# Performance work log

Hardware: AMD Instinct MI355X
Metric: run time of the kernel (lower is better)

The kernel has to match this reference:

```python
import jax, jax.numpy as jnp
import numpy as np

NUM_CLASSES = 100
CACHE_SIZE = 50
N_PROTOS = NUM_CLASSES * CACHE_SIZE  # 5000
FEAT_DIM = 128
BATCH = 2048
NVIEWS = 2
TEMP = 0.1
EPSILON = 0.05
PROTO_M = 0.99
TOPK = 10
LAMBDA_PCON = 1.0
SINKHORN_ITERS = 3


def _l1norm(x, axis):
    return x / jnp.clip(jnp.sum(jnp.abs(x), axis=axis, keepdims=True), 1e-12)


def _l2norm(x, axis=-1):
    return x / jnp.clip(jnp.linalg.norm(x, axis=axis, keepdims=True), 1e-12)


def _sinkhorn(feats, protos):
    # torch uses out.detach(): Q carries no gradient
    out = jax.lax.stop_gradient(feats @ protos.T)  # [N, K]
    Q = jnp.exp(out / EPSILON).T                   # [K, N]
    K_, B_ = Q.shape
    Q = Q / jnp.sum(Q)
    for _ in range(SINKHORN_ITERS):
        Q = _l1norm(Q, axis=1) / K_   # row L1 normalize
        Q = _l1norm(Q, axis=0) / B_   # col L1 normalize
    return (Q * B_).T                 # [N, K]


def _topk_mask(x, k):
    _, idx = jax.lax.top_k(x, k)
    rows = jnp.arange(x.shape[0])[:, None]
    return jnp.zeros_like(x).at[rows, idx].set(1.0)


def reference(features, targets, beta, protos):
    # features: [B, V, D] -> [V*B, D] (view-major, matches torch.cat(torch.unbind(dim=1)))
    feats = jnp.transpose(features, (1, 0, 2)).reshape(-1, FEAT_DIM)
    labels = jnp.tile(targets, NVIEWS)                              # [N]
    contrast_labels = jnp.tile(jnp.arange(NUM_CLASSES), CACHE_SIZE)  # [K]
    mask = (labels[:, None] == contrast_labels[None, :]).astype(feats.dtype)  # [N, K]

    # ---- mle_loss ----
    Q = _sinkhorn(feats, jax.lax.stop_gradient(protos))
    update_mask = mask * Q
    tkm = _topk_mask(update_mask, TOPK)
    update_mask = _l1norm(tkm * update_mask, axis=1)

    update_features = update_mask.T @ feats                         # [K, D]
    protos_new = PROTO_M * protos + (1.0 - PROTO_M) * update_features
    sim_mean = jax.lax.stop_gradient(
        jnp.mean(jnp.sum(_l2norm(update_features, 1) * _l2norm(protos, 1), axis=1)))
    protos2 = _l2norm(protos_new, axis=1)

    Q2 = _sinkhorn(feats, jax.lax.stop_gradient(protos2))
    logits = jax.nn.softplus(feats @ jax.lax.stop_gradient(protos2).T / TEMP)  # [N, K]

    loss_mask = mask * Q2
    # NOTE: original code top-ks update_mask (already normalized) here, not loss_mask
    tkm2 = _topk_mask(update_mask, TOPK)
    loss_mask = _l1norm(tkm2 * loss_mask, axis=1)
    masked_logits = loss_mask * logits

    positive_logits = mask * logits
    negative_logits = logits * (1.0 - mask)
    imp = jax.lax.stop_gradient(jnp.exp(beta * jnp.log(negative_logits + 1e-10)))
    total_logits = positive_logits + imp * negative_logits

    pos = jnp.sum(masked_logits, axis=1)                             # [N]
    neg = jnp.log(jnp.sum(jnp.exp(total_logits), axis=1, keepdims=True))  # [N, 1]
    # faithful to the torch broadcast: [N] - [N,1] -> [N, N]
    mle = -jnp.mean(pos - neg)

    # ---- proto_contra ----
    pn = _l2norm(protos2, axis=1)                                    # [K, D]
    plabels = jnp.tile(jnp.arange(NUM_CLASSES), CACHE_SIZE)
    pmask = (plabels[:, None] == plabels[None, :]).astype(pn.dtype)
    tau = jax.lax.stop_gradient((1.0 + (0.5 - sim_mean)) * 0.4)
    adc = pn @ pn.T / tau
    lg = adc - jax.lax.stop_gradient(jnp.max(adc, axis=1, keepdims=True))
    lmask = 1.0 - jnp.eye(N_PROTOS, dtype=pn.dtype)
    pmask = pmask * lmask
    ppos = jnp.sum(_l1norm(pmask, axis=1) * lg, axis=1)
    pneg = jnp.log(jnp.sum(lmask * jnp.exp(lg), axis=1))
    pcon = -jnp.mean(ppos - pneg)

    return mle + LAMBDA_PCON * pcon


def setup_inputs() -> dict:
    key = jax.random.key(0)
    k1, k2, k3 = jax.random.split(key, 3)
    features = jax.random.normal(k1, (BATCH, NVIEWS, FEAT_DIM), dtype=jnp.float32)
    features = _l2norm(features, axis=-1)  # unit-norm embeddings keep exp(./eps) finite
    targets = jax.random.randint(k2, (BATCH,), 0, NUM_CLASSES)
    beta = jnp.float32(0.5)
    protos = _l2norm(jax.random.uniform(k3, (N_PROTOS, FEAT_DIM), dtype=jnp.float32), axis=-1)
    return {"features": features, "targets": targets, "beta": beta, "protos": protos}
```

## Files before the change

kernel.cpp:

```cpp
#include <hip/hip_runtime.h>
#include <math.h>

constexpr int NUM_CLASSES = 100;
constexpr int CACHE_SIZE  = 50;
constexpr int NPROT       = 5000;
constexpr int FD          = 128;
constexpr int BATCH       = 2048;
constexpr int NROWS       = 4096;
constexpr int TOPK        = 10;
constexpr float INV_TEMP  = 10.0f;
constexpr float PROTO_M   = 0.99f;
constexpr int PLD         = 5120;
constexpr int SROWS       = 16;
constexpr int NSLOT       = NROWS / SROWS;
constexpr int NTILE       = 40;
constexpr int NTRI        = NTILE * (NTILE + 1) / 2;


typedef __attribute__((ext_vector_type(8))) short bf16x8;
typedef __attribute__((ext_vector_type(4))) float f32x4;
typedef __attribute__((ext_vector_type(4))) _Float16 f16x4;
typedef __attribute__((ext_vector_type(8))) _Float16 f16x8;

__device__ __forceinline__ float blockReduceSum(float v) {
  __shared__ float tmp[8];
  const int lane = threadIdx.x & 63;
  const int wid  = threadIdx.x >> 6;
  #pragma unroll
  for (int o = 32; o > 0; o >>= 1) v += __shfl_down(v, o, 64);
  __syncthreads();
  if (lane == 0) tmp[wid] = v;
  __syncthreads();
  const int nw = (blockDim.x + 63) >> 6;
  float s = 0.f;
  for (int i = 0; i < nw; ++i) s += tmp[i];
  return s;
}

__device__ __forceinline__ short f2bf(float x) {
  union { float f; unsigned u; } v; v.f = x;
  const unsigned r = v.u + 0x7fffu + ((v.u >> 16) & 1u);
  return (short)(r >> 16);
}

__global__ __launch_bounds__(1024) void k_build_prep(
    const float* __restrict__ features, const float* __restrict__ protos,
    const int* __restrict__ targets,
    float* __restrict__ feats, short* __restrict__ fb, short* __restrict__ pb,
    int* __restrict__ classbase, int* __restrict__ rowlist) {
  constexpr int NF4 = NROWS * (FD / 4);
  constexpr int NP4 = NPROT * FD / 4;
  __shared__ int t[BATCH];
  __shared__ short chcnt[8][NUM_CLASSES];
  __shared__ int   chpre[8][NUM_CLASSES];
  __shared__ int   ctot[NUM_CLASSES];
  __shared__ int   base[NUM_CLASSES + 1];
  if (blockIdx.x < 285) {
    const int w = blockIdx.x * 1024 + threadIdx.x;
    if (w < NF4) {
      const int n  = w >> 5;
      const int d4 = (w & 31) << 2;
      const int b  = n & (BATCH - 1);
      const int v  = n >> 11;
      const float4 src = *reinterpret_cast<const float4*>(features + ((size_t)b * 2 + v) * FD + d4);
      *reinterpret_cast<float4*>(feats + (size_t)n * FD + d4) = src;
      short4 h;
      h.x = f2bf(src.x); h.y = f2bf(src.y); h.z = f2bf(src.z); h.w = f2bf(src.w);
      *reinterpret_cast<short4*>(fb + (size_t)n * FD + d4) = h;
    } else if (w - NF4 < NP4) {
      const int u = w - NF4;
      const float4 v = *reinterpret_cast<const float4*>(protos + (size_t)u * 4);
      short4 h;
      h.x = f2bf(v.x); h.y = f2bf(v.y); h.z = f2bf(v.z); h.w = f2bf(v.w);
      *reinterpret_cast<short4*>(pb + (size_t)u * 4) = h;
    }
    return;
  }
  for (int i = threadIdx.x; i < BATCH; i += 1024) t[i] = targets[i];
  __syncthreads();
  if (threadIdx.x < 8 * NUM_CLASSES) {
    const int ch = threadIdx.x / NUM_CLASSES;
    const int c  = threadIdx.x % NUM_CLASSES;
    int m = 0;
    const int i0 = ch << 8;
    for (int i = i0; i < i0 + 256; ++i) m += (t[i] == c);
    chcnt[ch][c] = (short)m;
  }
  __syncthreads();
  if (threadIdx.x < NUM_CLASSES) {
    const int c = threadIdx.x;
    int s = 0;
    #pragma unroll
    for (int ch = 0; ch < 8; ++ch) { chpre[ch][c] = s; s += chcnt[ch][c]; }
    ctot[c] = s;
  }
  __syncthreads();
  if (threadIdx.x == 0) {
    int s = 0;
    for (int c = 0; c < NUM_CLASSES; ++c) { base[c] = s; s += 2 * ctot[c]; }
    base[NUM_CLASSES] = s;
  }
  __syncthreads();
  if (threadIdx.x <= NUM_CLASSES) classbase[threadIdx.x] = base[threadIdx.x];
  for (int b = threadIdx.x; b < BATCH; b += 1024) {
    const int c  = t[b];
    const int ch = b >> 8;
    int r = chpre[ch][c];
    for (int i = ch << 8; i < b; ++i) r += (t[i] == c);
    const int bs  = base[c];
    const int cnt = (base[c + 1] - bs) >> 1;
    rowlist[bs + r] = b;
    rowlist[bs + cnt + r] = BATCH + b;
  }
}

__global__ __launch_bounds__(256) void k_gemm_mfma(
    const short* __restrict__ A, const short* __restrict__ B,
    int Nb, _Float16* __restrict__ C, float* __restrict__ colpart) {
  __shared__ __align__(16) short Bs[128 * 64];
  __shared__ float red[4][128];
  const int tid  = threadIdx.x;
  const int wid  = tid >> 6;
  const int lane = tid & 63;
  const int lr   = lane & 15;
  const int kg   = lane >> 4;
  const int m0   = blockIdx.y * 128 + wid * 32;
  const int n0   = blockIdx.x * 128;

  f32x4 acc[2][8];
  #pragma unroll
  for (int i = 0; i < 2; ++i)
    #pragma unroll
    for (int j = 0; j < 8; ++j) acc[i][j] = (f32x4){0.f, 0.f, 0.f, 0.f};

  bool cval[8];
  #pragma unroll
  for (int j = 0; j < 8; ++j) cval[j] = (n0 + j * 16 + lr < Nb);

  const int scol = tid >> 1;
  const int sk   = (tid & 1) * 32;
  const int gcol = min(n0 + scol, Nb - 1);

  #pragma unroll
  for (int h = 0; h < 2; ++h) {
    const int k0 = h * 64;
    if (h) __syncthreads();
    #pragma unroll
    for (int u = 0; u < 4; ++u) {
      const int kk2 = sk + u * 8;
      const bf16x8 vb = *reinterpret_cast<const bf16x8*>(B + (size_t)gcol * FD + k0 + kk2);
      const int byteoff = (scol * 128 + kk2 * 2) ^ ((scol & 7) << 4);
      *reinterpret_cast<bf16x8*>(reinterpret_cast<char*>(&Bs[0]) + byteoff) = vb;
    }
    __syncthreads();
    #pragma unroll
    for (int kk = 0; kk < 2; ++kk) {
      const int kb = k0 + kk * 32 + kg * 8;
      bf16x8 av[2], bv[8];
      #pragma unroll
      for (int i = 0; i < 2; ++i)
        av[i] = *reinterpret_cast<const bf16x8*>(A + (size_t)(m0 + i * 16 + lr) * FD + kb);
      #pragma unroll
      for (int j = 0; j < 8; ++j) {
        const int col = j * 16 + lr;
        const int bo = (col * 128 + (kk * 32 + kg * 8) * 2) ^ ((col & 7) << 4);
        bv[j] = *reinterpret_cast<const bf16x8*>(reinterpret_cast<const char*>(&Bs[0]) + bo);
      }
      #pragma unroll
      for (int i = 0; i < 2; ++i)
        #pragma unroll
        for (int j = 0; j < 8; ++j)
          acc[i][j] = __builtin_amdgcn_mfma_f32_16x16x32_bf16(av[i], bv[j], acc[i][j], 0, 0, 0);
    }
  }

  float csum[8];
  #pragma unroll
  for (int j = 0; j < 8; ++j) csum[j] = 0.f;
  #pragma unroll
  for (int i = 0; i < 2; ++i) {
    const int rbase = m0 + i * 16 + kg * 4;
    #pragma unroll
    for (int j = 0; j < 8; ++j) {
      if (!cval[j]) continue;
      const int col = n0 + j * 16 + lr;
      #pragma unroll
      for (int q = 0; q < 4; ++q) {
        const float tval = __expf(acc[i][j][q] * INV_TEMP);
        const _Float16 tf = (_Float16)tval;
        C[(size_t)(rbase + q) * NPROT + col] = tf;
        const float t32 = (float)tf;
        csum[j] = fmaf(t32, t32, csum[j]);
      }
    }
  }
  __syncthreads();
  #pragma unroll
  for (int j = 0; j < 8; ++j) {
    float v = csum[j];
    v += __shfl_xor(v, 16, 64);
    v += __shfl_xor(v, 32, 64);
    if (lane < 16) red[wid][j * 16 + lane] = v;
  }
  __syncthreads();
  if (tid < 128) {
    const int col = n0 + tid;
    if (col < Nb) {
      const float t = red[0][tid] + red[1][tid] + red[2][tid] + red[3][tid];
      colpart[(size_t)blockIdx.y * PLD + col] = t;
    }
  }
}

template <bool WITH_MLE>
__global__ __launch_bounds__(1024) void k_sink_fused(const _Float16* __restrict__ big,
                                                     const float* __restrict__ Rin,
                                                     float* __restrict__ part,
                                                     float* __restrict__ semain,
                                                     const float* __restrict__ beta_ptr) {
  __shared__ float Cl[SROWS];
  const int r0   = blockIdx.x * SROWS;
  const int wid  = threadIdx.x >> 6;
  const int lane = threadIdx.x & 63;
  float beta = 0.f;
  bool bhalf = false;
  if constexpr (WITH_MLE) {
    beta = beta_ptr[0];
    bhalf = (beta == 0.5f);
  }
  {
    const int r = wid;
    const _Float16* row = big + (size_t)(r0 + r) * NPROT;
    float s = 0.f, se = 0.f;
    for (int idx = lane; idx < NPROT / 8; idx += 64) {
      const f16x8 v = *reinterpret_cast<const f16x8*>(row + idx * 8);
      const float4 q0 = *reinterpret_cast<const float4*>(Rin + idx * 8);
      const float4 q1 = *reinterpret_cast<const float4*>(Rin + idx * 8 + 4);
      float rt[8], rq[8];
      #pragma unroll
      for (int e = 0; e < 8; ++e) rt[e] = (float)v[e];
      rq[0] = q0.x; rq[1] = q0.y; rq[2] = q0.z; rq[3] = q0.w;
      rq[4] = q1.x; rq[5] = q1.y; rq[6] = q1.z; rq[7] = q1.w;
      #pragma unroll
      for (int e = 0; e < 8; ++e)
        s = fmaf(rt[e] * rt[e], rq[e], s);
      if constexpr (WITH_MLE) {
        #pragma unroll
        for (int e = 0; e < 8; ++e) {
          const float l = __logf(1.f + rt[e]);
          const float lb = l + 1e-10f;
          const float imp = bhalf ? sqrtf(lb) : __expf(beta * __logf(lb));
          se += __expf(imp * l);
        }
      }
    }
    #pragma unroll
    for (int o = 32; o > 0; o >>= 1) {
      s += __shfl_down(s, o, 64);
      if constexpr (WITH_MLE) se += __shfl_down(se, o, 64);
    }
    if (lane == 0) {
      Cl[r] = 1.0f / s;
      if constexpr (WITH_MLE) semain[r0 + r] = se;
    }
  }
  __syncthreads();
  for (int k4 = threadIdx.x * 4; k4 < NPROT; k4 += 4096) {
    float s[4] = {0.f, 0.f, 0.f, 0.f};
    #pragma unroll
    for (int r = 0; r < SROWS; ++r) {
      const f16x4 v = *reinterpret_cast<const f16x4*>(big + (size_t)(r0 + r) * NPROT + k4);
      const float c = Cl[r];
      #pragma unroll
      for (int e = 0; e < 4; ++e) {
        const float t = (float)v[e];
        s[e] = fmaf(t * t, c, s[e]);
      }
    }
    *reinterpret_cast<float4*>(part + (size_t)blockIdx.x * PLD + k4) =
        make_float4(s[0], s[1], s[2], s[3]);
  }
}

__global__ __launch_bounds__(512) void k_red_slots(const float* __restrict__ part,
                                                   int nslots, float* __restrict__ R) {
  __shared__ float red[8][64];
  const int g  = threadIdx.x >> 6;
  const int kk = threadIdx.x & 63;
  const int k  = blockIdx.x * 64 + kk;
  float s = 0.f;
  if (k < NPROT) {
    const int per = nslots >> 3;
    const int b0 = g * per, b1 = b0 + per;
    for (int b = b0; b < b1; ++b) s += part[(size_t)b * PLD + k];
  }
  red[g][kk] = s;
  __syncthreads();
  if (threadIdx.x < 64 && k < NPROT) {
    float t = 0.f;
    #pragma unroll
    for (int g2 = 0; g2 < 8; ++g2) t += red[g2][kk];
    R[k] = 1.0f / t;
  }
}

__global__ __launch_bounds__(256) void k_top10(const _Float16* __restrict__ out1,
                                               const float* __restrict__ R3,
                                               const int* __restrict__ targets,
                                               float* __restrict__ wsel) {
  const int n = blockIdx.x * 4 + (threadIdx.x >> 6);
  const int lane = threadIdx.x & 63;
  const int c = targets[n & (BATCH - 1)];
  float cur = -1.0f, orig = -1.0f;
  if (lane < CACHE_SIZE) {
    const int k = c + lane * NUM_CLASSES;
    const float t = (float)out1[(size_t)n * NPROT + k];
    cur = t * t * R3[k];
    orig = cur;
  }
  float tvsum = 0.f;
  bool selme = false;
  #pragma unroll
  for (int i = 0; i < TOPK; ++i) {
    float bv = cur;
    int   bj = lane;
    #pragma unroll
    for (int o = 32; o > 0; o >>= 1) {
      const float ov = __shfl_xor(bv, o, 64);
      const int   oj = __shfl_xor(bj, o, 64);
      if (ov > bv || (ov == bv && oj < bj)) { bv = ov; bj = oj; }
    }
    tvsum += bv;
    if (lane == bj) { cur = -2.0f; selme = true; }
  }
  tvsum = fmaxf(tvsum, 1e-12f);
  if (lane < CACHE_SIZE)
    wsel[(size_t)n * CACHE_SIZE + lane] = selme ? orig / tvsum : 0.f;
}

__global__ __launch_bounds__(128) void k_ufpu(const float* __restrict__ feats,
                                              const float* __restrict__ wsel,
                                              const int* __restrict__ rowlist,
                                              const int* __restrict__ classbase,
                                              const float* __restrict__ protos,
                                              short* __restrict__ pnb,
                                              float* __restrict__ simbuf) {
  const int k = blockIdx.x;
  const int d = threadIdx.x;
  const int c = k % NUM_CLASSES;
  const int j = k / NUM_CLASSES;
  const int b0 = classbase[c], b1 = classbase[c + 1];
  float u = 0.f;
  for (int ii = b0; ii < b1; ++ii) {
    const int n = rowlist[ii];
    const float wv = wsel[(size_t)n * CACHE_SIZE + j];
    if (wv != 0.f) u = fmaf(wv, feats[(size_t)n * FD + d], u);
  }
  const float p = protos[(size_t)k * FD + d];
  const float pnew = PROTO_M * p + (1.0f - PROTO_M) * u;
  const float spp = blockReduceSum(p * p);
  const float suu = blockReduceSum(u * u);
  const float sup = blockReduceSum(u * p);
  const float snn = blockReduceSum(pnew * pnew);
  const float x = pnew / fmaxf(sqrtf(snn), 1e-12f);
  pnb[(size_t)k * FD + d] = f2bf(x);
  if (d == 0)
    simbuf[k] = sup / (fmaxf(sqrtf(suu), 1e-12f) * fmaxf(sqrtf(spp), 1e-12f));
}

__global__ void k_tau(const float* __restrict__ simbuf, float* __restrict__ scalars) {
  float s = 0.f;
  for (int k = threadIdx.x; k < NPROT; k += 256) s += simbuf[k];
  s = blockReduceSum(s);
  if (threadIdx.x == 0) {
    const float sim_mean = s / (float)NPROT;
    scalars[0] = (1.0f + (0.5f - sim_mean)) * 0.4f;
  }
}

__global__ __launch_bounds__(256) void k_mle_fin(const _Float16* __restrict__ out2,
                                                 const float* __restrict__ R3,
                                                 const int* __restrict__ targets,
                                                 const float* __restrict__ wsel,
                                                 const float* __restrict__ beta_ptr,
                                                 const float* __restrict__ semain,
                                                 float* __restrict__ rowres) {
  const int n = blockIdx.x * 4 + (threadIdx.x >> 6);
  const int lane = threadIdx.x & 63;
  const int c = targets[n & (BATCH - 1)];
  const float beta = beta_ptr[0];
  const bool bhalf = (beta == 0.5f);
  float corr = 0.f, swl = 0.f, sw = 0.f;
  if (lane < CACHE_SIZE) {
    const int k = c + lane * NUM_CLASSES;
    const float t = (float)out2[(size_t)n * NPROT + k];
    const float l = __logf(1.f + t);
    const float lb = l + 1e-10f;
    const float imp = bhalf ? sqrtf(lb) : __expf(beta * __logf(lb));
    corr = (1.f + t) - __expf(imp * l);
    if (wsel[(size_t)n * CACHE_SIZE + lane] > 0.f) {
      const float w2 = t * t * R3[k];
      swl = w2 * l;
      sw  = w2;
    }
  }
  #pragma unroll
  for (int o = 32; o > 0; o >>= 1) {
    corr += __shfl_down(corr, o, 64);
    swl  += __shfl_down(swl,  o, 64);
    sw   += __shfl_down(sw,   o, 64);
  }
  if (lane == 0)
    rowres[n] = __logf(semain[n] + corr) - swl / fmaxf(sw, 1e-12f);
}

__global__ __launch_bounds__(256) void k_pcon_mfma(
    const short* __restrict__ P, const float* __restrict__ scalars,
    float* __restrict__ part_neg, float* __restrict__ part_pos) {
  __shared__ __align__(16) short Bs[128 * 64];
  int tdec = blockIdx.x, by = 0;
  while (tdec >= NTILE - by) { tdec -= NTILE - by; ++by; }
  const int bx = by + tdec;
  const bool diag = (bx == by);

  const int tid  = threadIdx.x;
  const int wid  = tid >> 6;
  const int lane = tid & 63;
  const int lr   = lane & 15;
  const int kg   = lane >> 4;
  const int k0r  = by * 128 + wid * 32;
  const int l0   = bx * 128;
  const float invtau = 1.0f / scalars[0];

  f32x4 acc[2][8];
  #pragma unroll
  for (int i = 0; i < 2; ++i)
    #pragma unroll
    for (int j = 0; j < 8; ++j) acc[i][j] = (f32x4){0.f, 0.f, 0.f, 0.f};

  int rowa[2];
  #pragma unroll
  for (int i = 0; i < 2; ++i) {
    const int r = k0r + i * 16 + lr;
    rowa[i] = (r < NPROT) ? r : (NPROT - 1);
  }
  bool cval[8];
  #pragma unroll
  for (int j = 0; j < 8; ++j) cval[j] = (l0 + j * 16 + lr < NPROT);

  const int scol = tid >> 1;
  const int sk   = (tid & 1) * 32;
  const int gcol = min(l0 + scol, NPROT - 1);

  #pragma unroll
  for (int h = 0; h < 2; ++h) {
    const int k0 = h * 64;
    if (h) __syncthreads();
    #pragma unroll
    for (int u = 0; u < 4; ++u) {
      const int kk2 = sk + u * 8;
      const bf16x8 vb = *reinterpret_cast<const bf16x8*>(P + (size_t)gcol * FD + k0 + kk2);
      const int byteoff = (scol * 128 + kk2 * 2) ^ ((scol & 7) << 4);
      *reinterpret_cast<bf16x8*>(reinterpret_cast<char*>(&Bs[0]) + byteoff) = vb;
    }
    __syncthreads();
    #pragma unroll
    for (int kk = 0; kk < 2; ++kk) {
      const int kb = k0 + kk * 32 + kg * 8;
      bf16x8 av[2], bv[8];
      #pragma unroll
      for (int i = 0; i < 2; ++i)
        av[i] = *reinterpret_cast<const bf16x8*>(P + (size_t)rowa[i] * FD + kb);
      #pragma unroll
      for (int j = 0; j < 8; ++j) {
        const int col = j * 16 + lr;
        const int bo = (col * 128 + (kk * 32 + kg * 8) * 2) ^ ((col & 7) << 4);
        bv[j] = *reinterpret_cast<const bf16x8*>(reinterpret_cast<const char*>(&Bs[0]) + bo);
      }
      #pragma unroll
      for (int i = 0; i < 2; ++i)
        #pragma unroll
        for (int j = 0; j < 8; ++j)
          acc[i][j] = __builtin_amdgcn_mfma_f32_16x16x32_bf16(av[i], bv[j], acc[i][j], 0, 0, 0);
    }
  }

  int ccls[8];
  #pragma unroll
  for (int j = 0; j < 8; ++j) ccls[j] = (l0 + j * 16 + lr) % NUM_CLASSES;
  float cneg[8], cpos[8];
  #pragma unroll
  for (int j = 0; j < 8; ++j) { cneg[j] = 0.f; cpos[j] = 0.f; }

  #pragma unroll
  for (int i = 0; i < 2; ++i) {
    float sneg[4] = {0.f, 0.f, 0.f, 0.f};
    float spos[4] = {0.f, 0.f, 0.f, 0.f};
    const int rbase = k0r + i * 16 + kg * 4;
    #pragma unroll
    for (int q = 0; q < 4; ++q) {
      const int rg = rbase + q;
      if (rg >= NPROT) continue;
      const int rcls = rg % NUM_CLASSES;
      #pragma unroll
      for (int j = 0; j < 8; ++j) {
        const int cg = l0 + j * 16 + lr;
        if (!cval[j]) continue;
        if (diag && cg == rg) continue;
        const float lg = fmaf(acc[i][j][q], invtau, -invtau);
        const float e  = __expf(lg);
        sneg[q] += e;
        cneg[j] += e;
        if (ccls[j] == rcls) { spos[q] += lg; cpos[j] += lg; }
      }
    }
    #pragma unroll
    for (int q = 0; q < 4; ++q) {
      float sn = sneg[q], sp = spos[q];
      #pragma unroll
      for (int off = 8; off > 0; off >>= 1) {
        sn += __shfl_xor(sn, off, 64);
        sp += __shfl_xor(sp, off, 64);
      }
      if (lr == 0) {
        const int rg = rbase + q;
        if (rg < NPROT) {
          part_neg[(size_t)bx * PLD + rg] = sn;
          part_pos[(size_t)bx * PLD + rg] = sp;
        }
      }
    }
  }

  if (!diag) {
    __syncthreads();
    float* redn = reinterpret_cast<float*>(&Bs[0]);
    float* redp = redn + 512;
    #pragma unroll
    for (int j = 0; j < 8; ++j) {
      float cn = cneg[j];
      cn += __shfl_xor(cn, 16, 64);
      cn += __shfl_xor(cn, 32, 64);
      float cp = cpos[j];
      cp += __shfl_xor(cp, 16, 64);
      cp += __shfl_xor(cp, 32, 64);
      if (lane < 16) {
        redn[wid * 128 + j * 16 + lane] = cn;
        redp[wid * 128 + j * 16 + lane] = cp;
      }
    }
    __syncthreads();
    if (tid < 128) {
      const int cg = l0 + tid;
      if (cg < NPROT) {
        const float tn = redn[tid] + redn[128 + tid] + redn[256 + tid] + redn[384 + tid];
        const float tp = redp[tid] + redp[128 + tid] + redp[256 + tid] + redp[384 + tid];
        part_neg[(size_t)by * PLD + cg] = tn;
        part_pos[(size_t)by * PLD + cg] = tp;
      }
    }
  }
}

__global__ __launch_bounds__(256) void k_pcon_fin(const float* __restrict__ part_neg,
                                                  const float* __restrict__ part_pos,
                                                  float* __restrict__ pconbuf) {
  __shared__ float rn[4][64], rp[4][64];
  const int g  = threadIdx.x >> 6;
  const int kk = threadIdx.x & 63;
  const int k  = blockIdx.x * 64 + kk;
  float sn = 0.f, sp = 0.f;
  if (k < NPROT) {
    for (int b = g * 10; b < g * 10 + 10; ++b) {
      sn += part_neg[(size_t)b * PLD + k];
      sp += part_pos[(size_t)b * PLD + k];
    }
  }
  rn[g][kk] = sn; rp[g][kk] = sp;
  __syncthreads();
  if (threadIdx.x < 64 && k < NPROT) {
    const float tn = rn[0][kk] + rn[1][kk] + rn[2][kk] + rn[3][kk];
    const float tp = rp[0][kk] + rp[1][kk] + rp[2][kk] + rp[3][kk];
    pconbuf[k] = __logf(tn) - tp * (1.0f / (float)(CACHE_SIZE - 1));
  }
}

__global__ void k_final(const float* __restrict__ rowres,
                        const float* __restrict__ pconbuf,
                        float* __restrict__ outp) {
  float s1 = 0.f, s2 = 0.f;
  for (int i = threadIdx.x; i < NROWS; i += 256) s1 += rowres[i];
  for (int i = threadIdx.x; i < NPROT; i += 256) s2 += pconbuf[i];
  s1 = blockReduceSum(s1);
  s2 = blockReduceSum(s2);
  if (threadIdx.x == 0) outp[0] = s1 / (float)NROWS + s2 / (float)NPROT;
}

extern "C" void kernel_launch(void* const* d_in, const int* in_sizes, int n_in,
                              void* d_out, int out_size, void* d_ws, size_t ws_size,
                              hipStream_t stream) {
  (void)in_sizes; (void)n_in; (void)out_size; (void)ws_size;
  const float* features = (const float*)d_in[0];
  const int*   targets  = (const int*)d_in[1];
  const float* beta     = (const float*)d_in[2];
  const float* protos   = (const float*)d_in[3];
  float* outp = (float*)d_out;

  char* basep = (char*)d_ws;
  size_t off = 0;
  auto alloc = [&](size_t bytes) -> void* {
    void* p = basep + off;
    off = (off + bytes + 255) & ~(size_t)255;
    return p;
  };
  _Float16* big  = (_Float16*)alloc((size_t)NROWS * NPROT * 2);
  float* feats   = (float*)alloc((size_t)NROWS * FD * 4);
  short* fb      = (short*)alloc((size_t)NROWS * FD * 2);
  short* pb      = (short*)alloc((size_t)NPROT * FD * 2);
  float* part    = (float*)alloc((size_t)NSLOT * PLD * 4);
  float* Rk      = (float*)alloc(NPROT * 4);
  float* wsel    = (float*)alloc((size_t)NROWS * CACHE_SIZE * 4);
  int*   rowlist = (int*)alloc(NROWS * 4);
  int*   classbase = (int*)alloc((NUM_CLASSES + 1) * 4);
  float* simbuf  = (float*)alloc(NPROT * 4);
  float* scalars = (float*)alloc(64);
  float* semain  = (float*)alloc(NROWS * 4);
  float* rowres  = (float*)alloc(NROWS * 4);
  float* pconbuf = (float*)alloc(NPROT * 4);
  float* pneg    = (float*)alloc((size_t)NTILE * PLD * 4);
  float* ppos    = (float*)alloc((size_t)NTILE * PLD * 4);

  k_build_prep<<<286, 1024, 0, stream>>>(features, protos, targets,
                                         feats, fb, pb, classbase, rowlist);

  k_gemm_mfma<<<dim3(40, 32), 256, 0, stream>>>(fb, pb, NPROT, big, part);
  k_red_slots<<<79, 512, 0, stream>>>(part, 32, Rk);
  k_sink_fused<false><<<NSLOT, 1024, 0, stream>>>(big, Rk, part, nullptr, nullptr);
  k_red_slots<<<79, 512, 0, stream>>>(part, NSLOT, Rk);
  k_sink_fused<false><<<NSLOT, 1024, 0, stream>>>(big, Rk, part, nullptr, nullptr);
  k_red_slots<<<79, 512, 0, stream>>>(part, NSLOT, Rk);

  k_top10<<<NROWS / 4, 256, 0, stream>>>(big, Rk, targets, wsel);
  k_ufpu<<<NPROT, 128, 0, stream>>>(feats, wsel, rowlist, classbase, protos, pb, simbuf);
  k_tau<<<1, 256, 0, stream>>>(simbuf, scalars);

  k_gemm_mfma<<<dim3(40, 32), 256, 0, stream>>>(fb, pb, NPROT, big, part);
  k_red_slots<<<79, 512, 0, stream>>>(part, 32, Rk);
  k_sink_fused<false><<<NSLOT, 1024, 0, stream>>>(big, Rk, part, nullptr, nullptr);
  k_red_slots<<<79, 512, 0, stream>>>(part, NSLOT, Rk);
  k_sink_fused<true><<<NSLOT, 1024, 0, stream>>>(big, Rk, part, semain, beta);
  k_red_slots<<<79, 512, 0, stream>>>(part, NSLOT, Rk);

  k_mle_fin<<<NROWS / 4, 256, 0, stream>>>(big, Rk, targets, wsel, beta, semain, rowres);
  k_pcon_mfma<<<NTRI, 256, 0, stream>>>(pb, scalars, pneg, ppos);
  k_pcon_fin<<<79, 256, 0, stream>>>(pneg, ppos, pconbuf);
  k_final<<<1, 256, 0, stream>>>(rowres, pconbuf, outp);
}
```

Baseline: 266.0 us.

## Write compact per-class exp tile in GEMM epilogue and fold tau into pcon

The GEMM epilogue now also stores the 50 same-class exp values per row into a dense [rows x 64] fp16 buffer. top10 and mle_fin then read this buffer instead of gathering with a stride of 100 across the full 4096x5000 matrix. The single-block tau kernel is removed, and each pcon block recomputes the sim_mean reduction over 5000 entries itself. This trades scattered gathers and one launch for extra conditional stores in the GEMM and redundant per-block reductions in pcon.

```diff
diff --git a/kernel.cpp b/kernel.cpp
--- a/kernel.cpp
+++ b/kernel.cpp
@@ -15,6 +15,7 @@
 constexpr int NSLOT       = NROWS / SROWS;
 constexpr int NTILE       = 40;
 constexpr int NTRI        = NTILE * (NTILE + 1) / 2;
+constexpr int CLD         = 64;
 
 
 typedef __attribute__((ext_vector_type(8))) short bf16x8;
@@ -116,7 +117,9 @@
 
 __global__ __launch_bounds__(256) void k_gemm_mfma(
     const short* __restrict__ A, const short* __restrict__ B,
-    int Nb, _Float16* __restrict__ C, float* __restrict__ colpart) {
+    const int* __restrict__ targets,
+    int Nb, _Float16* __restrict__ C, float* __restrict__ colpart,
+    _Float16* __restrict__ compact) {
   __shared__ __align__(16) short Bs[128 * 64];
   __shared__ float red[4][128];
   const int tid  = threadIdx.x;
@@ -174,6 +177,20 @@
     }
   }
 
+  int ccls[8], cdiv[8];
+  #pragma unroll
+  for (int j = 0; j < 8; ++j) {
+    const int col = n0 + j * 16 + lr;
+    ccls[j] = col % NUM_CLASSES;
+    cdiv[j] = col / NUM_CLASSES;
+  }
+  int rcls[2][4];
+  #pragma unroll
+  for (int i = 0; i < 2; ++i)
+    #pragma unroll
+    for (int q = 0; q < 4; ++q)
+      rcls[i][q] = targets[(m0 + i * 16 + kg * 4 + q) & (BATCH - 1)];
+
   float csum[8];
   #pragma unroll
   for (int j = 0; j < 8; ++j) csum[j] = 0.f;
@@ -189,6 +206,8 @@
         const float tval = __expf(acc[i][j][q] * INV_TEMP);
         const _Float16 tf = (_Float16)tval;
         C[(size_t)(rbase + q) * NPROT + col] = tf;
+        if (ccls[j] == rcls[i][q])
+          compact[(size_t)(rbase + q) * CLD + cdiv[j]] = tf;
         const float t32 = (float)tf;
         csum[j] = fmaf(t32, t32, csum[j]);
       }
@@ -304,7 +323,7 @@
   }
 }
 
-__global__ __launch_bounds__(256) void k_top10(const _Float16* __restrict__ out1,
+__global__ __launch_bounds__(256) void k_top10(const _Float16* __restrict__ compact,
                                                const float* __restrict__ R3,
                                                const int* __restrict__ targets,
                                                float* __restrict__ wsel) {
@@ -313,9 +332,8 @@
   const int c = targets[n & (BATCH - 1)];
   float cur = -1.0f, orig = -1.0f;
   if (lane < CACHE_SIZE) {
-    const int k = c + lane * NUM_CLASSES;
-    const float t = (float)out1[(size_t)n * NPROT + k];
-    cur = t * t * R3[k];
+    const float t = (float)compact[(size_t)n * CLD + lane];
+    cur = t * t * R3[c + lane * NUM_CLASSES];
     orig = cur;
   }
   float tvsum = 0.f;
@@ -368,17 +386,7 @@
     simbuf[k] = sup / (fmaxf(sqrtf(suu), 1e-12f) * fmaxf(sqrtf(spp), 1e-12f));
 }
 
-__global__ void k_tau(const float* __restrict__ simbuf, float* __restrict__ scalars) {
-  float s = 0.f;
-  for (int k = threadIdx.x; k < NPROT; k += 256) s += simbuf[k];
-  s = blockReduceSum(s);
-  if (threadIdx.x == 0) {
-    const float sim_mean = s / (float)NPROT;
-    scalars[0] = (1.0f + (0.5f - sim_mean)) * 0.4f;
-  }
-}
-
-__global__ __launch_bounds__(256) void k_mle_fin(const _Float16* __restrict__ out2,
+__global__ __launch_bounds__(256) void k_mle_fin(const _Float16* __restrict__ compact,
                                                  const float* __restrict__ R3,
                                                  const int* __restrict__ targets,
                                                  const float* __restrict__ wsel,
@@ -392,14 +400,13 @@
   const bool bhalf = (beta == 0.5f);
   float corr = 0.f, swl = 0.f, sw = 0.f;
   if (lane < CACHE_SIZE) {
-    const int k = c + lane * NUM_CLASSES;
-    const float t = (float)out2[(size_t)n * NPROT + k];
+    const float t = (float)compact[(size_t)n * CLD + lane];
     const float l = __logf(1.f + t);
     const float lb = l + 1e-10f;
     const float imp = bhalf ? sqrtf(lb) : __expf(beta * __logf(lb));
     corr = (1.f + t) - __expf(imp * l);
     if (wsel[(size_t)n * CACHE_SIZE + lane] > 0.f) {
-      const float w2 = t * t * R3[k];
+      const float w2 = t * t * R3[c + lane * NUM_CLASSES];
       swl = w2 * l;
       sw  = w2;
     }
@@ -415,7 +422,7 @@
 }
 
 __global__ __launch_bounds__(256) void k_pcon_mfma(
-    const short* __restrict__ P, const float* __restrict__ scalars,
+    const short* __restrict__ P, const float* __restrict__ simbuf,
     float* __restrict__ part_neg, float* __restrict__ part_pos) {
   __shared__ __align__(16) short Bs[128 * 64];
   int tdec = blockIdx.x, by = 0;
@@ -430,7 +437,12 @@
   const int kg   = lane >> 4;
   const int k0r  = by * 128 + wid * 32;
   const int l0   = bx * 128;
-  const float invtau = 1.0f / scalars[0];
+
+  float ssim = 0.f;
+  for (int k = tid; k < NPROT; k += 256) ssim += simbuf[k];
+  ssim = blockReduceSum(ssim);
+  const float sim_mean = ssim / (float)NPROT;
+  const float invtau = 1.0f / ((1.0f + (0.5f - sim_mean)) * 0.4f);
 
   f32x4 acc[2][8];
   #pragma unroll
@@ -455,7 +467,7 @@
   #pragma unroll
   for (int h = 0; h < 2; ++h) {
     const int k0 = h * 64;
-    if (h) __syncthreads();
+    __syncthreads();
     #pragma unroll
     for (int u = 0; u < 4; ++u) {
       const int kk2 = sk + u * 8;
@@ -614,6 +626,7 @@
     return p;
   };
   _Float16* big  = (_Float16*)alloc((size_t)NROWS * NPROT * 2);
+  _Float16* compact = (_Float16*)alloc((size_t)NROWS * CLD * 2);
   float* feats   = (float*)alloc((size_t)NROWS * FD * 4);
   short* fb      = (short*)alloc((size_t)NROWS * FD * 2);
   short* pb      = (short*)alloc((size_t)NPROT * FD * 2);
@@ -623,7 +636,6 @@
   int*   rowlist = (int*)alloc(NROWS * 4);
   int*   classbase = (int*)alloc((NUM_CLASSES + 1) * 4);
   float* simbuf  = (float*)alloc(NPROT * 4);
-  float* scalars = (float*)alloc(64);
   float* semain  = (float*)alloc(NROWS * 4);
   float* rowres  = (float*)alloc(NROWS * 4);
   float* pconbuf = (float*)alloc(NPROT * 4);
@@ -633,26 +645,25 @@
   k_build_prep<<<286, 1024, 0, stream>>>(features, protos, targets,
                                          feats, fb, pb, classbase, rowlist);
 
-  k_gemm_mfma<<<dim3(40, 32), 256, 0, stream>>>(fb, pb, NPROT, big, part);
+  k_gemm_mfma<<<dim3(40, 32), 256, 0, stream>>>(fb, pb, targets, NPROT, big, part, compact);
   k_red_slots<<<79, 512, 0, stream>>>(part, 32, Rk);
   k_sink_fused<false><<<NSLOT, 1024, 0, stream>>>(big, Rk, part, nullptr, nullptr);
   k_red_slots<<<79, 512, 0, stream>>>(part, NSLOT, Rk);
   k_sink_fused<false><<<NSLOT, 1024, 0, stream>>>(big, Rk, part, nullptr, nullptr);
   k_red_slots<<<79, 512, 0, stream>>>(part, NSLOT, Rk);
 
-  k_top10<<<NROWS / 4, 256, 0, stream>>>(big, Rk, targets, wsel);
+  k_top10<<<NROWS / 4, 256, 0, stream>>>(compact, Rk, targets, wsel);
   k_ufpu<<<NPROT, 128, 0, stream>>>(feats, wsel, rowlist, classbase, protos, pb, simbuf);
-  k_tau<<<1, 256, 0, stream>>>(simbuf, scalars);
-
-  k_gemm_mfma<<<dim3(40, 32), 256, 0, stream>>>(fb, pb, NPROT, big, part);
+
+  k_gemm_mfma<<<dim3(40, 32), 256, 0, stream>>>(fb, pb, targets, NPROT, big, part, compact);
   k_red_slots<<<79, 512, 0, stream>>>(part, 32, Rk);
   k_sink_fused<false><<<NSLOT, 1024, 0, stream>>>(big, Rk, part, nullptr, nullptr);
   k_red_slots<<<79, 512, 0, stream>>>(part, NSLOT, Rk);
   k_sink_fused<true><<<NSLOT, 1024, 0, stream>>>(big, Rk, part, semain, beta);
   k_red_slots<<<79, 512, 0, stream>>>(part, NSLOT, Rk);
 
-  k_mle_fin<<<NROWS / 4, 256, 0, stream>>>(big, Rk, targets, wsel, beta, semain, rowres);
-  k_pcon_mfma<<<NTRI, 256, 0, stream>>>(pb, scalars, pneg, ppos);
+  k_mle_fin<<<NROWS / 4, 256, 0, stream>>>(compact, Rk, targets, wsel, beta, semain, rowres);
+  k_pcon_mfma<<<NTRI, 256, 0, stream>>>(pb, simbuf, pneg, ppos);
   k_pcon_fin<<<79, 256, 0, stream>>>(pneg, ppos, pconbuf);
   k_final<<<1, 256, 0, stream>>>(rowres, pconbuf, outp);
 }
```

Result: no change. 264.9 us (-0.4%).
